# Optimization experiments

Measured on AMD Instinct MI355X. Metric: run time of the kernel, lower is better.

The kernel has to match this reference:

```python
import jax, jax.numpy as jnp
import numpy as np

B, N, D, H, O, K, N_USER, C = 1, 4096, 64, 4, 64, 2, 4000, 2


def setup_inputs() -> dict:
    key = jax.random.key(0)
    ks = jax.random.split(key, 7)
    h = jax.random.normal(ks[0], (B, N, D), jnp.float32)
    # dense 0/1 adjacency per heterogeneous kind, with self-loops so no row is empty
    adj = jax.random.randint(ks[1], (K, B, N, N), 0, 2).astype(jnp.float32)
    hadj = jnp.maximum(adj, jnp.eye(N, dtype=jnp.float32))
    s = 1.0 / np.sqrt(D).astype(np.float32)
    w = jax.random.normal(ks[2], (K, H, D, O), jnp.float32) * s
    a_src = jax.random.normal(ks[3], (K, H, O, 1), jnp.float32) * (1.0 / np.sqrt(O).astype(np.float32))
    a_dst = jax.random.normal(ks[4], (K, H, O, 1), jnp.float32) * (1.0 / np.sqrt(O).astype(np.float32))
    fc_w = jax.random.normal(ks[5], (C, O * K), jnp.float32) * (1.0 / np.sqrt(O * K).astype(np.float32))
    fc_b = jnp.zeros((C,), jnp.float32)
    return {"h": h, "hadj": hadj, "w": w, "a_src": a_src, "a_dst": a_dst, "fc_w": fc_w, "fc_b": fc_b}


def _gat(h, adj, w_k, a_src_k, a_dst_k):
    # h: (B,N,D); adj: (B,N,N); w_k: (H,D,O); a_*: (H,O,1)
    h_prime = jnp.einsum('bnf,hfo->bhno', h, w_k)          # (B,H,N,O)
    t = jnp.tanh(h_prime)
    attn_src = jnp.einsum('bhno,hoi->bhni', t, a_src_k)    # (B,H,N,1)
    attn_dst = jnp.einsum('bhno,hoi->bhni', t, a_dst_k)    # (B,H,N,1)
    attn = attn_src + jnp.swapaxes(attn_dst, -1, -2)       # (B,H,N,N) broadcast add
    attn = jnp.where(attn >= 0, attn, 0.2 * attn)          # LeakyReLU(0.2)
    attn = jnp.where(adj[:, None] > 0, attn, -jnp.inf)     # dense mask
    attn = jax.nn.softmax(attn, axis=-1)                   # dropout is a no-op in eval
    out = jnp.einsum('bhnm,bhmo->bhno', attn, h_prime)     # (B,H,N,O)
    return out.mean(axis=1)                                # mean over heads -> (B,N,O)


def reference(h, hadj, w, a_src, a_dst, fc_w, fc_b):
    embs = []
    for k in range(K):  # small fixed loop over heterogeneous node kinds
        x = _gat(h, hadj[k], w[k], a_src[k], a_dst[k])
        embs.append(x[:, :N_USER])
    type_aware = jnp.concatenate(embs, axis=-1)            # (B, N_USER, K*O)
    logits = type_aware @ fc_w.T + fc_b                    # (B, N_USER, C)
    return jax.nn.log_softmax(logits, axis=-1)
```

## Files before the change

### kernel.cpp

```cpp
#include <hip/hip_runtime.h>
#include <math.h>

constexpr int KK = 2;
constexpr int HH = 4;
constexpr int NN = 4096;
constexpr int DD = 64;
constexpr int OO = 64;
constexpr int NU = 4000;
constexpr int CC = 2;
constexpr int JSPLIT = 16;
constexpr int JCHUNK = NN / JSPLIT;
constexpr float LOG2E = 1.44269504088896340736f;

typedef float vf4 __attribute__((ext_vector_type(4)));
typedef float vf2 __attribute__((ext_vector_type(2)));

__device__ __forceinline__ float fexp2(float x) {
#if __has_builtin(__builtin_amdgcn_exp2f)
  return __builtin_amdgcn_exp2f(x);
#else
  return exp2f(x);
#endif
}
__device__ __forceinline__ float frcp(float x) {
#if __has_builtin(__builtin_amdgcn_rcpf)
  return __builtin_amdgcn_rcpf(x);
#else
  return 1.0f / x;
#endif
}
__device__ __forceinline__ float ftanh(float x) {
  float e = fexp2(x * (2.0f * LOG2E));
  return 1.0f - 2.0f * frcp(e + 1.0f);
}

__global__ __launch_bounds__(256) void gat_phase1(
    const float* __restrict__ hsrc, const float* __restrict__ w,
    const float* __restrict__ a_src, const float* __restrict__ a_dst,
    const float* __restrict__ fc_w,
    float* __restrict__ srcAA, float* __restrict__ bb5,
    float* __restrict__ gg) {
  const int kh = blockIdx.y;
  const int k = kh >> 2;
  const int i0 = blockIdx.x * 64;
  const int tid = threadIdx.x;

  __shared__ float h_s[DD][68];
  __shared__ float w_s[DD][OO];
  __shared__ float part[4][64][17];

  {
    const vf4* wp = (const vf4*)(w + (size_t)kh * DD * OO);
    vf4* ws4 = (vf4*)w_s;
    for (int t = tid; t < DD * OO / 4; t += 256) ws4[t] = wp[t];
  }
  for (int t = tid; t < 1024; t += 256) {
    const int row = t >> 4;
    const int f4 = (t & 15) * 4;
    vf4 v = *(const vf4*)(hsrc + (size_t)(i0 + row) * DD + f4);
    h_s[f4 + 0][row] = v.x;
    h_s[f4 + 1][row] = v.y;
    h_s[f4 + 2][row] = v.z;
    h_s[f4 + 3][row] = v.w;
  }
  __syncthreads();

  const int og = tid & 15;
  const int rg = tid >> 4;
  const int o0 = og * 4;
  const int r0 = rg * 4;

  float hp[4][4];
#pragma unroll
  for (int j = 0; j < 4; ++j)
#pragma unroll
    for (int u = 0; u < 4; ++u) hp[j][u] = 0.0f;

#pragma unroll 8
  for (int f = 0; f < DD; ++f) {
    vf4 hv = *(const vf4*)&h_s[f][r0];
    vf4 wv = *(const vf4*)&w_s[f][o0];
    hp[0][0] = fmaf(hv.x, wv.x, hp[0][0]);
    hp[0][1] = fmaf(hv.x, wv.y, hp[0][1]);
    hp[0][2] = fmaf(hv.x, wv.z, hp[0][2]);
    hp[0][3] = fmaf(hv.x, wv.w, hp[0][3]);
    hp[1][0] = fmaf(hv.y, wv.x, hp[1][0]);
    hp[1][1] = fmaf(hv.y, wv.y, hp[1][1]);
    hp[1][2] = fmaf(hv.y, wv.z, hp[1][2]);
    hp[1][3] = fmaf(hv.y, wv.w, hp[1][3]);
    hp[2][0] = fmaf(hv.z, wv.x, hp[2][0]);
    hp[2][1] = fmaf(hv.z, wv.y, hp[2][1]);
    hp[2][2] = fmaf(hv.z, wv.z, hp[2][2]);
    hp[2][3] = fmaf(hv.z, wv.w, hp[2][3]);
    hp[3][0] = fmaf(hv.w, wv.x, hp[3][0]);
    hp[3][1] = fmaf(hv.w, wv.y, hp[3][1]);
    hp[3][2] = fmaf(hv.w, wv.z, hp[3][2]);
    hp[3][3] = fmaf(hv.w, wv.w, hp[3][3]);
  }

  float as[4], ad[4], f0[4], f1[4];
#pragma unroll
  for (int u = 0; u < 4; ++u) {
    as[u] = a_src[kh * OO + o0 + u];
    ad[u] = a_dst[kh * OO + o0 + u];
    f0[u] = fc_w[0 * (KK * OO) + k * OO + o0 + u];
    f1[u] = fc_w[1 * (KK * OO) + k * OO + o0 + u];
  }

#pragma unroll
  for (int j = 0; j < 4; ++j) {
    float sp = 0.0f, dp = 0.0f, g0 = 0.0f, g1 = 0.0f;
#pragma unroll
    for (int u = 0; u < 4; ++u) {
      float v = hp[j][u];
      float t = ftanh(v);
      sp = fmaf(t, as[u], sp);
      dp = fmaf(t, ad[u], dp);
      g0 = fmaf(v, f0[u], g0);
      g1 = fmaf(v, f1[u], g1);
    }
    part[0][r0 + j][og] = sp;
    part[1][r0 + j][og] = dp;
    part[2][r0 + j][og] = g0;
    part[3][r0 + j][og] = g1;
  }
  __syncthreads();

  {
    const int val = tid & 3;
    const int j2 = tid >> 2;
    const float* pr = &part[val][j2][0];
    vf4 s0 = *(const vf4*)(pr + 0);
    vf4 s1 = *(const vf4*)(pr + 4);
    vf4 s2 = *(const vf4*)(pr + 8);
    vf4 s3 = *(const vf4*)(pr + 12);
    vf4 t4 = s0 + s1 + s2 + s3;
    float sum = t4.x + t4.y + t4.z + t4.w;
    const size_t idx = (size_t)kh * NN + i0 + j2;
    if (val == 0) {
      float sp = sum * LOG2E;
      vf2 v = {fexp2(sp), fexp2(0.2f * sp)};
      *(vf2*)(srcAA + idx * 2) = v;
    } else if (val == 1) {
      float dp = sum * LOG2E;
      vf2 v = {fexp2(dp), fexp2(0.2f * dp)};
      *(vf2*)(bb5 + idx * 2) = v;
    } else {
      gg[idx * 2 + (val - 2)] = sum;
    }
  }
}

__global__ __launch_bounds__(256) void gat_phase2(
    const float* __restrict__ adj, const float* __restrict__ srcAA,
    const float* __restrict__ bb5, const float* __restrict__ gg,
    float* __restrict__ P) {
  const int k = blockIdx.y >> 4;
  const int chunk = blockIdx.y & 15;
  const int r0 = blockIdx.x * 16;
  const int tid = threadIdx.x;
  const int wave = tid >> 6;
  const int lane = tid & 63;
  const int row = lane & 15;
  const int jsub = lane >> 4;
  const int i = r0 + row;
  const int j0 = chunk * JCHUNK;

  __shared__ float lds_bb[HH][JCHUNK * 2];
  __shared__ float lds_gg[HH][JCHUNK * 2];

#pragma unroll
  for (int step = 0; step < 4; ++step) {
    const int idx = step * 256 + tid;
    const int sel = idx >> 9;
    const int h = (idx >> 7) & 3;
    const int pos = (idx & 127) * 4;
    const float* src =
        (sel ? gg : bb5) + ((size_t)(k * HH + h) * NN + j0) * 2 + pos;
    vf4 v = *(const vf4*)src;
    if (sel)
      *(vf4*)&lds_gg[h][pos] = v;
    else
      *(vf4*)&lds_bb[h][pos] = v;
  }

  vf2 AA[4];
#pragma unroll
  for (int h = 0; h < 4; ++h)
    AA[h] = *(const vf2*)(srcAA + ((size_t)(k * HH + h) * NN + i) * 2);

  float l[4], a0[4], a1[4];
#pragma unroll
  for (int h = 0; h < 4; ++h) {
    l[h] = 0.0f;
    a0[h] = 0.0f;
    a1[h] = 0.0f;
  }

  __syncthreads();

  const float* arow =
      adj + (size_t)k * NN * NN + (size_t)i * NN + j0 + jsub * 4;
  vf4 aj[4];
#pragma unroll
  for (int q = 0; q < 4; ++q)
    aj[q] = *(const vf4*)(arow + (wave + q * 4) * 16);

#pragma unroll
  for (int s = 0; s < 4; ++s) {
    const int t = wave + s * 4;
    const vf4 av = aj[s];
    const int jl = (t * 16 + jsub * 4) * 2;
#pragma unroll
    for (int h = 0; h < 4; ++h) {
      vf4 b01 = *(const vf4*)&lds_bb[h][jl];
      vf4 b23 = *(const vf4*)&lds_bb[h][jl + 4];
      vf4 g01 = *(const vf4*)&lds_gg[h][jl];
      vf4 g23 = *(const vf4*)&lds_gg[h][jl + 4];
      vf2 bp[4] = {{b01.x, b01.y}, {b01.z, b01.w}, {b23.x, b23.y}, {b23.z, b23.w}};
      vf2 gp[4] = {{g01.x, g01.y}, {g01.z, g01.w}, {g23.x, g23.y}, {g23.z, g23.w}};
#pragma unroll
      for (int jj = 0; jj < 4; ++jj) {
        vf2 PP = AA[h] * bp[jj];
        float e = fmaxf(PP.x, PP.y);
        float pa = e * av[jj];
        l[h] += pa;
        a0[h] = fmaf(pa, gp[jj].x, a0[h]);
        a1[h] = fmaf(pa, gp[jj].y, a1[h]);
      }
    }
  }

#pragma unroll
  for (int h = 0; h < 4; ++h) {
    l[h] += __shfl_xor(l[h], 16, 64);
    l[h] += __shfl_xor(l[h], 32, 64);
    a0[h] += __shfl_xor(a0[h], 16, 64);
    a0[h] += __shfl_xor(a0[h], 32, 64);
    a1[h] += __shfl_xor(a1[h], 16, 64);
    a1[h] += __shfl_xor(a1[h], 32, 64);
  }

  __shared__ float sred[4][12][16];
  if (lane < 16) {
#pragma unroll
    for (int h = 0; h < 4; ++h) {
      sred[wave][h * 3 + 0][row] = l[h];
      sred[wave][h * 3 + 1][row] = a0[h];
      sred[wave][h * 3 + 2][row] = a1[h];
    }
  }
  __syncthreads();
  if (tid < 192) {
    const int v = tid >> 4;
    const int rr = tid & 15;
    float sum =
        sred[0][v][rr] + sred[1][v][rr] + sred[2][v][rr] + sred[3][v][rr];
    const int h = v / 3, c = v % 3;
    size_t base =
        ((((size_t)(k * JSPLIT + chunk) * HH + h) * 3 + c)) * NU + (r0 + rr);
    P[base] = sum;
  }
}

__global__ __launch_bounds__(256) void gat_phase3(
    const float* __restrict__ P, const float* __restrict__ fc_b,
    float* __restrict__ out) {
  const int i = blockIdx.x * 256 + threadIdx.x;
  if (i >= NU) return;
  float l0 = fc_b[0], l1 = fc_b[1];
#pragma unroll
  for (int k = 0; k < KK; ++k) {
#pragma unroll
    for (int q = 0; q < HH; ++q) {
      float ls = 0.0f, a0 = 0.0f, a1 = 0.0f;
#pragma unroll
      for (int ch = 0; ch < JSPLIT; ++ch) {
        size_t b = (((size_t)(k * JSPLIT + ch) * HH + q) * 3) * NU + i;
        ls += P[b];
        a0 += P[b + NU];
        a1 += P[b + 2 * (size_t)NU];
      }
      float inv = 1.0f / ls;
      l0 = fmaf(0.25f * a0, inv, l0);
      l1 = fmaf(0.25f * a1, inv, l1);
    }
  }
  float m = fmaxf(l0, l1);
  float lse = m + logf(expf(l0 - m) + expf(l1 - m));
  out[i * CC + 0] = l0 - lse;
  out[i * CC + 1] = l1 - lse;
}

extern "C" void kernel_launch(void* const* d_in, const int* in_sizes, int n_in,
                              void* d_out, int out_size, void* d_ws, size_t ws_size,
                              hipStream_t stream) {
  const float* hsrc  = (const float*)d_in[0];
  const float* hadj  = (const float*)d_in[1];
  const float* w     = (const float*)d_in[2];
  const float* a_src = (const float*)d_in[3];
  const float* a_dst = (const float*)d_in[4];
  const float* fc_w  = (const float*)d_in[5];
  const float* fc_b  = (const float*)d_in[6];
  float* out = (float*)d_out;

  char* ws = (char*)d_ws;
  float* srcAA = (float*)(ws + 0);
  float* bb5   = (float*)(ws + 262144);
  float* gg    = (float*)(ws + 524288);
  float* P     = (float*)(ws + 786432);

  dim3 g1(NN / 64, KK * HH);
  gat_phase1<<<g1, 256, 0, stream>>>(hsrc, w, a_src, a_dst, fc_w,
                                     srcAA, bb5, gg);
  dim3 g2(NU / 16, KK * JSPLIT);
  gat_phase2<<<g2, 256, 0, stream>>>(hadj, srcAA, bb5, gg, P);
  gat_phase3<<<(NU + 255) / 256, 256, 0, stream>>>(P, fc_b, out);
}
```

Measured before the change: 222.0 us.

## Process full adjacency rows per block with packed-vector math and in-block normalization

Phase 2 now gives each block four whole rows across all columns, instead of a 16-row by 256-column chunk. Per-column B/B5/g0/g1 values are read directly from global memory in a planar layout rather than staged through LDS. Accumulation uses packed two-wide vector max/fma, and the per-head normalization and head-mean happen inside the block, so phase 3 only sums two values. This removes the large split-J partial buffer and the LDS staging. In exchange it relies on cache for the per-column vectors, which each block now reloads for every row group, and the grid has fewer blocks (2000).

```diff
diff --git a/kernel.cpp b/kernel.cpp
--- a/kernel.cpp
+++ b/kernel.cpp
@@ -8,8 +8,6 @@
 constexpr int OO = 64;
 constexpr int NU = 4000;
 constexpr int CC = 2;
-constexpr int JSPLIT = 16;
-constexpr int JCHUNK = NN / JSPLIT;
 constexpr float LOG2E = 1.44269504088896340736f;
 
 typedef float vf4 __attribute__((ext_vector_type(4)));
@@ -38,8 +36,9 @@
     const float* __restrict__ hsrc, const float* __restrict__ w,
     const float* __restrict__ a_src, const float* __restrict__ a_dst,
     const float* __restrict__ fc_w,
-    float* __restrict__ srcAA, float* __restrict__ bb5,
-    float* __restrict__ gg) {
+    float* __restrict__ srcAA, float* __restrict__ Bp,
+    float* __restrict__ B5p, float* __restrict__ g0p,
+    float* __restrict__ g1p) {
   const int kh = blockIdx.y;
   const int k = kh >> 2;
   const int i0 = blockIdx.x * 64;
@@ -143,149 +142,143 @@
       *(vf2*)(srcAA + idx * 2) = v;
     } else if (val == 1) {
       float dp = sum * LOG2E;
-      vf2 v = {fexp2(dp), fexp2(0.2f * dp)};
-      *(vf2*)(bb5 + idx * 2) = v;
+      Bp[idx] = fexp2(dp);
+      B5p[idx] = fexp2(0.2f * dp);
+    } else if (val == 2) {
+      g0p[idx] = sum;
     } else {
-      gg[idx * 2 + (val - 2)] = sum;
+      g1p[idx] = sum;
     }
   }
 }
 
 __global__ __launch_bounds__(256) void gat_phase2(
     const float* __restrict__ adj, const float* __restrict__ srcAA,
-    const float* __restrict__ bb5, const float* __restrict__ gg,
-    float* __restrict__ P) {
-  const int k = blockIdx.y >> 4;
-  const int chunk = blockIdx.y & 15;
-  const int r0 = blockIdx.x * 16;
+    const float* __restrict__ Bp, const float* __restrict__ B5p,
+    const float* __restrict__ g0p, const float* __restrict__ g1p,
+    float* __restrict__ S) {
+  const int k = blockIdx.y;
+  const int r0 = blockIdx.x * 4;
   const int tid = threadIdx.x;
   const int wave = tid >> 6;
   const int lane = tid & 63;
-  const int row = lane & 15;
-  const int jsub = lane >> 4;
-  const int i = r0 + row;
-  const int j0 = chunk * JCHUNK;
-
-  __shared__ float lds_bb[HH][JCHUNK * 2];
-  __shared__ float lds_gg[HH][JCHUNK * 2];
-
-#pragma unroll
-  for (int step = 0; step < 4; ++step) {
-    const int idx = step * 256 + tid;
-    const int sel = idx >> 9;
-    const int h = (idx >> 7) & 3;
-    const int pos = (idx & 127) * 4;
-    const float* src =
-        (sel ? gg : bb5) + ((size_t)(k * HH + h) * NN + j0) * 2 + pos;
-    vf4 v = *(const vf4*)src;
-    if (sel)
-      *(vf4*)&lds_gg[h][pos] = v;
-    else
-      *(vf4*)&lds_bb[h][pos] = v;
-  }
-
-  vf2 AA[4];
-#pragma unroll
-  for (int h = 0; h < 4; ++h)
-    AA[h] = *(const vf2*)(srcAA + ((size_t)(k * HH + h) * NN + i) * 2);
-
-  float l[4], a0[4], a1[4];
+
+  float A[4][4], A5[4][4];
 #pragma unroll
   for (int h = 0; h < 4; ++h) {
-    l[h] = 0.0f;
-    a0[h] = 0.0f;
-    a1[h] = 0.0f;
-  }
-
+    const float* base = srcAA + ((size_t)(k * HH + h) * NN + r0) * 2;
+#pragma unroll
+    for (int r = 0; r < 4; ++r) {
+      A[r][h] = base[r * 2 + 0];
+      A5[r][h] = base[r * 2 + 1];
+    }
+  }
+
+  vf2 l2[4][4], a02[4][4], a12[4][4];
+#pragma unroll
+  for (int r = 0; r < 4; ++r)
+#pragma unroll
+    for (int h = 0; h < 4; ++h) {
+      l2[r][h] = (vf2)(0.0f);
+      a02[r][h] = (vf2)(0.0f);
+      a12[r][h] = (vf2)(0.0f);
+    }
+
+  const float* adjk = adj + (size_t)k * NN * NN;
+  const int jw = wave * 1024 + lane * 4;
+
+#pragma unroll 1
+  for (int t = 0; t < 4; ++t) {
+    const int j = jw + t * 256;
+    vf4 av[4];
+#pragma unroll
+    for (int r = 0; r < 4; ++r)
+      av[r] = *(const vf4*)(adjk + (size_t)(r0 + r) * NN + j);
+#pragma unroll
+    for (int h = 0; h < 4; ++h) {
+      const size_t pb = (size_t)(k * HH + h) * NN + j;
+      vf4 b = *(const vf4*)(Bp + pb);
+      vf4 b5 = *(const vf4*)(B5p + pb);
+      vf4 g0 = *(const vf4*)(g0p + pb);
+      vf4 g1 = *(const vf4*)(g1p + pb);
+      vf2 blo = {b.x, b.y}, bhi = {b.z, b.w};
+      vf2 b5lo = {b5.x, b5.y}, b5hi = {b5.z, b5.w};
+      vf2 g0lo = {g0.x, g0.y}, g0hi = {g0.z, g0.w};
+      vf2 g1lo = {g1.x, g1.y}, g1hi = {g1.z, g1.w};
+#pragma unroll
+      for (int r = 0; r < 4; ++r) {
+        vf2 alo = {av[r].x, av[r].y}, ahi = {av[r].z, av[r].w};
+        {
+          vf2 e = __builtin_elementwise_max(blo * A[r][h], b5lo * A5[r][h]);
+          vf2 pa = e * alo;
+          l2[r][h] += pa;
+          a02[r][h] = __builtin_elementwise_fma(pa, g0lo, a02[r][h]);
+          a12[r][h] = __builtin_elementwise_fma(pa, g1lo, a12[r][h]);
+        }
+        {
+          vf2 e = __builtin_elementwise_max(bhi * A[r][h], b5hi * A5[r][h]);
+          vf2 pa = e * ahi;
+          l2[r][h] += pa;
+          a02[r][h] = __builtin_elementwise_fma(pa, g0hi, a02[r][h]);
+          a12[r][h] = __builtin_elementwise_fma(pa, g1hi, a12[r][h]);
+        }
+      }
+    }
+  }
+
+  float red[4][4][3];
+#pragma unroll
+  for (int r = 0; r < 4; ++r)
+#pragma unroll
+    for (int h = 0; h < 4; ++h) {
+      float x0 = l2[r][h].x + l2[r][h].y;
+      float x1 = a02[r][h].x + a02[r][h].y;
+      float x2 = a12[r][h].x + a12[r][h].y;
+#pragma unroll
+      for (int off = 32; off > 0; off >>= 1) {
+        x0 += __shfl_xor(x0, off, 64);
+        x1 += __shfl_xor(x1, off, 64);
+        x2 += __shfl_xor(x2, off, 64);
+      }
+      red[r][h][0] = x0;
+      red[r][h][1] = x1;
+      red[r][h][2] = x2;
+    }
+
+  __shared__ float sred[4][48];
+  if (lane == 0) {
+#pragma unroll
+    for (int r = 0; r < 4; ++r)
+#pragma unroll
+      for (int h = 0; h < 4; ++h) {
+#pragma unroll
+        for (int c = 0; c < 3; ++c)
+          sred[wave][(r * 4 + h) * 3 + c] = red[r][h][c];
+      }
+  }
   __syncthreads();
-
-  const float* arow =
-      adj + (size_t)k * NN * NN + (size_t)i * NN + j0 + jsub * 4;
-  vf4 aj[4];
-#pragma unroll
-  for (int q = 0; q < 4; ++q)
-    aj[q] = *(const vf4*)(arow + (wave + q * 4) * 16);
-
-#pragma unroll
-  for (int s = 0; s < 4; ++s) {
-    const int t = wave + s * 4;
-    const vf4 av = aj[s];
-    const int jl = (t * 16 + jsub * 4) * 2;
+  if (tid < 8) {
+    const int r = tid >> 1, c = tid & 1;
+    float acc = 0.0f;
 #pragma unroll
     for (int h = 0; h < 4; ++h) {
-      vf4 b01 = *(const vf4*)&lds_bb[h][jl];
-      vf4 b23 = *(const vf4*)&lds_bb[h][jl + 4];
-      vf4 g01 = *(const vf4*)&lds_gg[h][jl];
-      vf4 g23 = *(const vf4*)&lds_gg[h][jl + 4];
-      vf2 bp[4] = {{b01.x, b01.y}, {b01.z, b01.w}, {b23.x, b23.y}, {b23.z, b23.w}};
-      vf2 gp[4] = {{g01.x, g01.y}, {g01.z, g01.w}, {g23.x, g23.y}, {g23.z, g23.w}};
-#pragma unroll
-      for (int jj = 0; jj < 4; ++jj) {
-        vf2 PP = AA[h] * bp[jj];
-        float e = fmaxf(PP.x, PP.y);
-        float pa = e * av[jj];
-        l[h] += pa;
-        a0[h] = fmaf(pa, gp[jj].x, a0[h]);
-        a1[h] = fmaf(pa, gp[jj].y, a1[h]);
-      }
-    }
-  }
-
-#pragma unroll
-  for (int h = 0; h < 4; ++h) {
-    l[h] += __shfl_xor(l[h], 16, 64);
-    l[h] += __shfl_xor(l[h], 32, 64);
-    a0[h] += __shfl_xor(a0[h], 16, 64);
-    a0[h] += __shfl_xor(a0[h], 32, 64);
-    a1[h] += __shfl_xor(a1[h], 16, 64);
-    a1[h] += __shfl_xor(a1[h], 32, 64);
-  }
-
-  __shared__ float sred[4][12][16];
-  if (lane < 16) {
-#pragma unroll
-    for (int h = 0; h < 4; ++h) {
-      sred[wave][h * 3 + 0][row] = l[h];
-      sred[wave][h * 3 + 1][row] = a0[h];
-      sred[wave][h * 3 + 2][row] = a1[h];
-    }
-  }
-  __syncthreads();
-  if (tid < 192) {
-    const int v = tid >> 4;
-    const int rr = tid & 15;
-    float sum =
-        sred[0][v][rr] + sred[1][v][rr] + sred[2][v][rr] + sred[3][v][rr];
-    const int h = v / 3, c = v % 3;
-    size_t base =
-        ((((size_t)(k * JSPLIT + chunk) * HH + h) * 3 + c)) * NU + (r0 + rr);
-    P[base] = sum;
+      const int vb = (r * 4 + h) * 3;
+      float ls = sred[0][vb] + sred[1][vb] + sred[2][vb] + sred[3][vb];
+      float ac = sred[0][vb + 1 + c] + sred[1][vb + 1 + c] +
+                 sred[2][vb + 1 + c] + sred[3][vb + 1 + c];
+      acc += ac / ls;
+    }
+    S[((size_t)k * NU + r0 + r) * CC + c] = 0.25f * acc;
   }
 }
 
 __global__ __launch_bounds__(256) void gat_phase3(
-    const float* __restrict__ P, const float* __restrict__ fc_b,
+    const float* __restrict__ S, const float* __restrict__ fc_b,
     float* __restrict__ out) {
   const int i = blockIdx.x * 256 + threadIdx.x;
   if (i >= NU) return;
-  float l0 = fc_b[0], l1 = fc_b[1];
-#pragma unroll
-  for (int k = 0; k < KK; ++k) {
-#pragma unroll
-    for (int q = 0; q < HH; ++q) {
-      float ls = 0.0f, a0 = 0.0f, a1 = 0.0f;
-#pragma unroll
-      for (int ch = 0; ch < JSPLIT; ++ch) {
-        size_t b = (((size_t)(k * JSPLIT + ch) * HH + q) * 3) * NU + i;
-        ls += P[b];
-        a0 += P[b + NU];
-        a1 += P[b + 2 * (size_t)NU];
-      }
-      float inv = 1.0f / ls;
-      l0 = fmaf(0.25f * a0, inv, l0);
-      l1 = fmaf(0.25f * a1, inv, l1);
-    }
-  }
+  float l0 = S[(size_t)i * CC + 0] + S[((size_t)NU + i) * CC + 0] + fc_b[0];
+  float l1 = S[(size_t)i * CC + 1] + S[((size_t)NU + i) * CC + 1] + fc_b[1];
   float m = fmaxf(l0, l1);
   float lse = m + logf(expf(l0 - m) + expf(l1 - m));
   out[i * CC + 0] = l0 - lse;
@@ -306,14 +299,16 @@
 
   char* ws = (char*)d_ws;
   float* srcAA = (float*)(ws + 0);
-  float* bb5   = (float*)(ws + 262144);
-  float* gg    = (float*)(ws + 524288);
-  float* P     = (float*)(ws + 786432);
+  float* Bp    = (float*)(ws + 262144);
+  float* B5p   = (float*)(ws + 393216);
+  float* g0p   = (float*)(ws + 524288);
+  float* g1p   = (float*)(ws + 655360);
+  float* S     = (float*)(ws + 786432);
 
   dim3 g1(NN / 64, KK * HH);
   gat_phase1<<<g1, 256, 0, stream>>>(hsrc, w, a_src, a_dst, fc_w,
-                                     srcAA, bb5, gg);
-  dim3 g2(NU / 16, KK * JSPLIT);
-  gat_phase2<<<g2, 256, 0, stream>>>(hadj, srcAA, bb5, gg, P);
-  gat_phase3<<<(NU + 255) / 256, 256, 0, stream>>>(P, fc_b, out);
-}
+                                     srcAA, Bp, B5p, g0p, g1p);
+  dim3 g2(NU / 4, KK);
+  gat_phase2<<<g2, 256, 0, stream>>>(hadj, srcAA, Bp, B5p, g0p, g1p, S);
+  gat_phase3<<<(NU + 255) / 256, 256, 0, stream>>>(S, fc_b, out);
+}
```

Result: slower. 231.5 us (+4.3%).
